# Kernel optimization log

Hardware: AMD Instinct MI355X
Metric: run time of the kernel (lower is better)

## Reference

```python
import jax, jax.numpy as jnp
import numpy as np

GRAVITY = 9.81
W_INERTIA = 1.0
W_GRAVITY = 0.01
W_STRAIN = 1.0

V = 500_000
E = 2_000_000


def setup_inputs() -> dict:
    key = jax.random.key(0)
    ks = jax.random.split(key, 7)
    pos_next = jax.random.normal(ks[0], (V, 3), dtype=jnp.float32)
    pos_curr = jax.random.normal(ks[1], (V, 3), dtype=jnp.float32)
    pos_prev = jax.random.normal(ks[2], (V, 3), dtype=jnp.float32)
    mass = jax.random.uniform(ks[3], (V, 1), dtype=jnp.float32)
    elements = jax.random.randint(ks[4], (E, 4), 0, V, dtype=jnp.int64)
    rest_volumes = jax.random.uniform(ks[5], (E,), dtype=jnp.float32)
    rest_inv = jax.random.normal(ks[6], (E, 3, 3), dtype=jnp.float32)
    lam = jnp.float32(1.0)
    mu = jnpp_one = jnp.float32(1.0)
    return {
        "pos_next": pos_next, "pos_curr": pos_curr, "pos_prev": pos_prev,
        "mass": mass, "elements": elements, "rest_volumes": rest_volumes,
        "rest_inv": rest_inv, "lam": lam, "mu": mu,
    }


def _det3(F):
    # F: (E, 3, 3)
    return (F[:, 0, 0] * (F[:, 1, 1] * F[:, 2, 2] - F[:, 1, 2] * F[:, 2, 1])
            - F[:, 0, 1] * (F[:, 1, 0] * F[:, 2, 2] - F[:, 1, 2] * F[:, 2, 0])
            + F[:, 0, 2] * (F[:, 1, 0] * F[:, 2, 1] - F[:, 1, 1] * F[:, 2, 0]))


def _physics_loss(pos_next, pos_curr, pos_prev, mass, elements, rest_volumes, rest_inv, lam, mu):
    # Inertia: mean over all V*3 entries of 0.5 * m * a^2
    accel = pos_next + pos_prev - 2.0 * pos_curr          # (V, 3)
    inertia = 0.5 * jnp.mean(mass * accel * accel)
    # Gravity: -mean(m * g * y)
    gravity = -jnp.mean(mass * GRAVITY * pos_curr[:, 1:2])
    # Strain (Neo-Hookean) on pos_next
    v = pos_next[elements]                                 # (E, 4, 3)
    Ds = jnp.stack([v[:, 1] - v[:, 0], v[:, 2] - v[:, 0], v[:, 3] - v[:, 0]], axis=-1)  # (E,3,3)
    F_def = jnp.einsum('eij,ejk->eik', Ds, rest_inv)       # (E, 3, 3)
    det_F = jnp.maximum(_det3(F_def), 1e-8)
    log_det = jnp.log(det_F)
    tr_FtF = jnp.sum(F_def * F_def, axis=(1, 2))           # trace(F^T F) = ||F||_F^2
    psi = 0.5 * lam * log_det ** 2 - mu * log_det + 0.5 * mu * (tr_FtF - 3.0)
    strain = jnp.mean(psi * rest_volumes)
    return W_INERTIA * inertia + W_GRAVITY * gravity + W_STRAIN * strain


def reference(pos_next, pos_curr, pos_prev, mass, elements, rest_volumes, rest_inv, lam, mu):
    return _physics_loss(pos_next, pos_curr, pos_prev, mass, elements, rest_volumes, rest_inv, lam, mu)
```

## Files before the change

### kernel.cpp

```cpp
#include <hip/hip_runtime.h>

#define GRAVITY_F 9.81f
#define EPT 2

typedef int   v4i  __attribute__((ext_vector_type(4)));
typedef float v4f  __attribute__((ext_vector_type(4), aligned(16)));
typedef float v4fu __attribute__((ext_vector_type(4), aligned(4)));

__device__ __forceinline__ float blockReduceSum(float val) {
    #pragma unroll
    for (int off = 32; off > 0; off >>= 1)
        val += __shfl_down(val, off, 64);
    __shared__ float smem[16];
    const int lane = threadIdx.x & 63;
    const int wave = threadIdx.x >> 6;
    if (lane == 0) smem[wave] = val;
    __syncthreads();
    const int nwaves = (blockDim.x + 63) >> 6;
    val = 0.0f;
    if (wave == 0) {
        if (lane < nwaves) val = smem[lane];
        #pragma unroll
        for (int off = 8; off > 0; off >>= 1)
            val += __shfl_down(val, off, 64);
    }
    return val;
}

__global__ void __launch_bounds__(256, 4)
fused_kernel(const float* __restrict__ pn,
             const float* __restrict__ pc,
             const float* __restrict__ pp,
             const float* __restrict__ mass,
             const int*   __restrict__ elems,
             const float* __restrict__ vols,
             const float* __restrict__ rinv,
             const float* __restrict__ lam_p,
             const float* __restrict__ mu_p,
             float* __restrict__ partials,
             int V, int E, int Vblocks4,
             float sI, float sG, float sS) {
    float local = 0.0f;

    if ((int)blockIdx.x >= Vblocks4) {
        const float lam = lam_p[0];
        const float mu  = mu_p[0];
        const int eb   = blockIdx.x - Vblocks4;
        const int base = eb * (EPT * 256) + threadIdx.x;

        int   ec[EPT];
        float sc[EPT];
        #pragma unroll
        for (int i = 0; i < EPT; ++i) {
            const int e = base + i * 256;
            ec[i] = e < E ? e : (E - 1);
            sc[i] = e < E ? sS : 0.0f;
        }

        v4i idx[EPT];
        #pragma unroll
        for (int i = 0; i < EPT; ++i)
            idx[i] = __builtin_nontemporal_load(((const v4i*)elems) + ec[i]);

        v4fu rA[EPT], rB[EPT];
        float rC[EPT], vol[EPT];
        #pragma unroll
        for (int i = 0; i < EPT; ++i) {
            const float* Rp = rinv + 9 * (size_t)ec[i];
            rA[i]  = __builtin_nontemporal_load((const v4fu*)Rp);
            rB[i]  = __builtin_nontemporal_load((const v4fu*)(Rp + 4));
            rC[i]  = __builtin_nontemporal_load(Rp + 8);
            vol[i] = __builtin_nontemporal_load(vols + ec[i]);
        }

        float x[EPT][4][3];
        #pragma unroll
        for (int i = 0; i < EPT; ++i) {
            const float* v0 = pn + 3 * (size_t)idx[i].x;
            const float* v1 = pn + 3 * (size_t)idx[i].y;
            const float* v2 = pn + 3 * (size_t)idx[i].z;
            const float* v3 = pn + 3 * (size_t)idx[i].w;
            #pragma unroll
            for (int r = 0; r < 3; ++r) {
                x[i][0][r] = v0[r];
                x[i][1][r] = v1[r];
                x[i][2][r] = v2[r];
                x[i][3][r] = v3[r];
            }
        }

        asm volatile("" ::
            "v"(x[0][0][0]), "v"(x[0][0][1]), "v"(x[0][0][2]),
            "v"(x[0][1][0]), "v"(x[0][1][1]), "v"(x[0][1][2]),
            "v"(x[0][2][0]), "v"(x[0][2][1]), "v"(x[0][2][2]),
            "v"(x[0][3][0]), "v"(x[0][3][1]), "v"(x[0][3][2]),
            "v"(x[1][0][0]), "v"(x[1][0][1]), "v"(x[1][0][2]),
            "v"(x[1][1][0]), "v"(x[1][1][1]), "v"(x[1][1][2]),
            "v"(x[1][2][0]), "v"(x[1][2][1]), "v"(x[1][2][2]),
            "v"(x[1][3][0]), "v"(x[1][3][1]), "v"(x[1][3][2]),
            "v"(rA[0]), "v"(rB[0]), "v"(rA[1]), "v"(rB[1]),
            "v"(rC[0]), "v"(rC[1]), "v"(vol[0]), "v"(vol[1]));

        #pragma unroll
        for (int i = 0; i < EPT; ++i) {
            const float R[9] = { rA[i][0], rA[i][1], rA[i][2], rA[i][3],
                                 rB[i][0], rB[i][1], rB[i][2], rB[i][3],
                                 rC[i] };
            float d[3][3];
            #pragma unroll
            for (int r = 0; r < 3; ++r) {
                d[r][0] = x[i][1][r] - x[i][0][r];
                d[r][1] = x[i][2][r] - x[i][0][r];
                d[r][2] = x[i][3][r] - x[i][0][r];
            }
            float F[3][3];
            #pragma unroll
            for (int r = 0; r < 3; ++r)
                #pragma unroll
                for (int k = 0; k < 3; ++k)
                    F[r][k] = d[r][0] * R[0 * 3 + k]
                            + d[r][1] * R[1 * 3 + k]
                            + d[r][2] * R[2 * 3 + k];
            const float det = F[0][0] * (F[1][1] * F[2][2] - F[1][2] * F[2][1])
                            - F[0][1] * (F[1][0] * F[2][2] - F[1][2] * F[2][0])
                            + F[0][2] * (F[1][0] * F[2][1] - F[1][1] * F[2][0]);
            const float ld = logf(fmaxf(det, 1e-8f));
            float tr = 0.0f;
            #pragma unroll
            for (int r = 0; r < 3; ++r)
                #pragma unroll
                for (int k = 0; k < 3; ++k)
                    tr += F[r][k] * F[r][k];
            const float psi = 0.5f * lam * ld * ld - mu * ld + 0.5f * mu * (tr - 3.0f);
            local += sc[i] * (psi * vol[i]);
        }
    } else {
        const int g  = blockIdx.x * blockDim.x + threadIdx.x;
        const int v0 = g * 4;
        if (v0 + 4 <= V) {
            const v4f m4 = *(const v4f*)(mass + v0);
            const v4f n0 = *(const v4f*)(pn + 3 * v0);
            const v4f n1 = *(const v4f*)(pn + 3 * v0 + 4);
            const v4f n2 = *(const v4f*)(pn + 3 * v0 + 8);
            const v4f c0 = __builtin_nontemporal_load((const v4f*)(pc + 3 * v0));
            const v4f c1 = __builtin_nontemporal_load((const v4f*)(pc + 3 * v0 + 4));
            const v4f c2 = __builtin_nontemporal_load((const v4f*)(pc + 3 * v0 + 8));
            const v4f q0 = __builtin_nontemporal_load((const v4f*)(pp + 3 * v0));
            const v4f q1 = __builtin_nontemporal_load((const v4f*)(pp + 3 * v0 + 4));
            const v4f q2 = __builtin_nontemporal_load((const v4f*)(pp + 3 * v0 + 8));
            const v4f N[3] = { n0, n1, n2 };
            const v4f C[3] = { c0, c1, c2 };
            const v4f Q[3] = { q0, q1, q2 };
            #pragma unroll
            for (int i = 0; i < 4; ++i) {
                float acc = 0.0f;
                #pragma unroll
                for (int r = 0; r < 3; ++r) {
                    const int k = 3 * i + r;
                    const float a = N[k >> 2][k & 3] + Q[k >> 2][k & 3]
                                  - 2.0f * C[k >> 2][k & 3];
                    acc += a * a;
                }
                const int ky = 3 * i + 1;
                const float y = C[ky >> 2][ky & 3];
                local += sI * (m4[i] * acc) + sG * (m4[i] * y);
            }
        } else {
            for (int v = v0; v < V; ++v) {
                const float m  = mass[v];
                const float p0 = pc[3 * v + 0];
                const float y  = pc[3 * v + 1];
                const float p2 = pc[3 * v + 2];
                const float a0 = pn[3 * v + 0] + pp[3 * v + 0] - 2.0f * p0;
                const float a1 = pn[3 * v + 1] + pp[3 * v + 1] - 2.0f * y;
                const float a2 = pn[3 * v + 2] + pp[3 * v + 2] - 2.0f * p2;
                local += sI * (m * (a0 * a0 + a1 * a1 + a2 * a2)) + sG * (m * y);
            }
        }
    }

    const float tot = blockReduceSum(local);
    if (threadIdx.x == 0) partials[blockIdx.x] = tot;
}

__global__ void reduce_kernel(const float* __restrict__ partials, int n,
                              float* __restrict__ out) {
    double s = 0.0;
    for (int i = threadIdx.x; i < n; i += blockDim.x)
        s += (double)partials[i];
    __shared__ double sm[256];
    sm[threadIdx.x] = s;
    __syncthreads();
    #pragma unroll
    for (int off = 128; off > 0; off >>= 1) {
        if (threadIdx.x < off) sm[threadIdx.x] += sm[threadIdx.x + off];
        __syncthreads();
    }
    if (threadIdx.x == 0) out[0] = (float)sm[0];
}

extern "C" void kernel_launch(void* const* d_in, const int* in_sizes, int n_in,
                              void* d_out, int out_size, void* d_ws, size_t ws_size,
                              hipStream_t stream) {
    const float* pos_next = (const float*)d_in[0];
    const float* pos_curr = (const float*)d_in[1];
    const float* pos_prev = (const float*)d_in[2];
    const float* mass     = (const float*)d_in[3];
    const int*   elements = (const int*)d_in[4];
    const float* rest_vol = (const float*)d_in[5];
    const float* rest_inv = (const float*)d_in[6];
    const float* lam_p    = (const float*)d_in[7];
    const float* mu_p     = (const float*)d_in[8];
    float* out = (float*)d_out;

    const int V = in_sizes[3];
    const int E = in_sizes[5];

    const float sI = 0.5f / (3.0f * (float)V);
    const float sG = -0.01f * GRAVITY_F / (float)V;
    const float sS = 1.0f / (float)E;

    const int block = 256;
    const int Eblocks  = (E + EPT * block - 1) / (EPT * block);
    const int Vgroups  = (V + 3) / 4;
    const int Vblocks4 = (Vgroups + block - 1) / block;
    const int grid = Vblocks4 + Eblocks;

    float* partials = (float*)d_ws;

    fused_kernel<<<grid, block, 0, stream>>>(pos_next, pos_curr, pos_prev,
                                             mass, elements, rest_vol,
                                             rest_inv, lam_p, mu_p,
                                             partials, V, E, Vblocks4,
                                             sI, sG, sS);
    reduce_kernel<<<1, 256, 0, stream>>>(partials, grid, out);
}
```

Measured before the change: 217.9 us.

## Process four contiguous elements per thread with aligned vector loads of rest_inv

Each thread now handles four consecutive elements, so the 36 rest_inv floats, four volumes and four index vectors can be read with fully aligned 16-byte nontemporal loads instead of misaligned per-element loads. Element blocks are placed before vertex blocks in the grid, and launch bounds drop to 3 waves per SIMD to make room for the larger register footprint. The gather of pos_next stays the same, but more gathers are in flight per thread. The cost is higher register pressure and lower occupancy, plus per-thread strided access across lanes, which may reduce coalescing.

```diff
diff --git a/kernel.cpp b/kernel.cpp
--- a/kernel.cpp
+++ b/kernel.cpp
@@ -1,11 +1,10 @@
 #include <hip/hip_runtime.h>
 
 #define GRAVITY_F 9.81f
-#define EPT 2
-
-typedef int   v4i  __attribute__((ext_vector_type(4)));
-typedef float v4f  __attribute__((ext_vector_type(4), aligned(16)));
-typedef float v4fu __attribute__((ext_vector_type(4), aligned(4)));
+#define EPT 4
+
+typedef int   v4i __attribute__((ext_vector_type(4)));
+typedef float v4f __attribute__((ext_vector_type(4), aligned(16)));
 
 __device__ __forceinline__ float blockReduceSum(float val) {
     #pragma unroll
@@ -27,7 +26,7 @@
     return val;
 }
 
-__global__ void __launch_bounds__(256, 4)
+__global__ void __launch_bounds__(256, 3)
 fused_kernel(const float* __restrict__ pn,
              const float* __restrict__ pc,
              const float* __restrict__ pp,
@@ -38,54 +37,65 @@
              const float* __restrict__ lam_p,
              const float* __restrict__ mu_p,
              float* __restrict__ partials,
-             int V, int E, int Vblocks4,
+             int V, int E, int Eblocks,
              float sI, float sG, float sS) {
     float local = 0.0f;
 
-    if ((int)blockIdx.x >= Vblocks4) {
+    if ((int)blockIdx.x < Eblocks) {
         const float lam = lam_p[0];
         const float mu  = mu_p[0];
-        const int eb   = blockIdx.x - Vblocks4;
-        const int base = eb * (EPT * 256) + threadIdx.x;
-
-        int   ec[EPT];
+        const int t  = blockIdx.x * 256 + threadIdx.x;
+        const int e0 = t * 4;
+
+        float rf[36];
+        v4i   idx[EPT];
+        float vol[EPT];
         float sc[EPT];
-        #pragma unroll
-        for (int i = 0; i < EPT; ++i) {
-            const int e = base + i * 256;
-            ec[i] = e < E ? e : (E - 1);
-            sc[i] = e < E ? sS : 0.0f;
-        }
-
-        v4i idx[EPT];
-        #pragma unroll
-        for (int i = 0; i < EPT; ++i)
-            idx[i] = __builtin_nontemporal_load(((const v4i*)elems) + ec[i]);
-
-        v4fu rA[EPT], rB[EPT];
-        float rC[EPT], vol[EPT];
-        #pragma unroll
-        for (int i = 0; i < EPT; ++i) {
-            const float* Rp = rinv + 9 * (size_t)ec[i];
-            rA[i]  = __builtin_nontemporal_load((const v4fu*)Rp);
-            rB[i]  = __builtin_nontemporal_load((const v4fu*)(Rp + 4));
-            rC[i]  = __builtin_nontemporal_load(Rp + 8);
-            vol[i] = __builtin_nontemporal_load(vols + ec[i]);
+
+        if (e0 + EPT <= E) {
+            v4f rq[9];
+            const v4f* Rp = (const v4f*)(rinv + 36 * (size_t)t);
+            #pragma unroll
+            for (int k = 0; k < 9; ++k)
+                rq[k] = __builtin_nontemporal_load(Rp + k);
+            const v4f vv = __builtin_nontemporal_load((const v4f*)(vols + 4 * (size_t)t));
+            #pragma unroll
+            for (int i = 0; i < EPT; ++i)
+                idx[i] = __builtin_nontemporal_load((const v4i*)elems + (4 * (size_t)t + i));
+            #pragma unroll
+            for (int k = 0; k < 9; ++k)
+                #pragma unroll
+                for (int j = 0; j < 4; ++j)
+                    rf[4 * k + j] = rq[k][j];
+            #pragma unroll
+            for (int i = 0; i < EPT; ++i) { vol[i] = vv[i]; sc[i] = sS; }
+        } else {
+            #pragma unroll
+            for (int i = 0; i < EPT; ++i) {
+                const int e  = e0 + i;
+                const int ec = e < E ? e : (E - 1);
+                sc[i]  = e < E ? sS : 0.0f;
+                vol[i] = __builtin_nontemporal_load(vols + ec);
+                idx[i] = __builtin_nontemporal_load((const v4i*)elems + ec);
+                #pragma unroll
+                for (int k = 0; k < 9; ++k)
+                    rf[9 * i + k] = __builtin_nontemporal_load(rinv + 9 * (size_t)ec + k);
+            }
         }
 
         float x[EPT][4][3];
         #pragma unroll
         for (int i = 0; i < EPT; ++i) {
-            const float* v0 = pn + 3 * (size_t)idx[i].x;
-            const float* v1 = pn + 3 * (size_t)idx[i].y;
-            const float* v2 = pn + 3 * (size_t)idx[i].z;
-            const float* v3 = pn + 3 * (size_t)idx[i].w;
+            const float* p0 = pn + 3 * (size_t)idx[i].x;
+            const float* p1 = pn + 3 * (size_t)idx[i].y;
+            const float* p2 = pn + 3 * (size_t)idx[i].z;
+            const float* p3 = pn + 3 * (size_t)idx[i].w;
             #pragma unroll
             for (int r = 0; r < 3; ++r) {
-                x[i][0][r] = v0[r];
-                x[i][1][r] = v1[r];
-                x[i][2][r] = v2[r];
-                x[i][3][r] = v3[r];
+                x[i][0][r] = p0[r];
+                x[i][1][r] = p1[r];
+                x[i][2][r] = p2[r];
+                x[i][3][r] = p3[r];
             }
         }
 
@@ -97,15 +107,30 @@
             "v"(x[1][0][0]), "v"(x[1][0][1]), "v"(x[1][0][2]),
             "v"(x[1][1][0]), "v"(x[1][1][1]), "v"(x[1][1][2]),
             "v"(x[1][2][0]), "v"(x[1][2][1]), "v"(x[1][2][2]),
-            "v"(x[1][3][0]), "v"(x[1][3][1]), "v"(x[1][3][2]),
-            "v"(rA[0]), "v"(rB[0]), "v"(rA[1]), "v"(rB[1]),
-            "v"(rC[0]), "v"(rC[1]), "v"(vol[0]), "v"(vol[1]));
+            "v"(x[1][3][0]), "v"(x[1][3][1]), "v"(x[1][3][2]));
+        asm volatile("" ::
+            "v"(x[2][0][0]), "v"(x[2][0][1]), "v"(x[2][0][2]),
+            "v"(x[2][1][0]), "v"(x[2][1][1]), "v"(x[2][1][2]),
+            "v"(x[2][2][0]), "v"(x[2][2][1]), "v"(x[2][2][2]),
+            "v"(x[2][3][0]), "v"(x[2][3][1]), "v"(x[2][3][2]),
+            "v"(x[3][0][0]), "v"(x[3][0][1]), "v"(x[3][0][2]),
+            "v"(x[3][1][0]), "v"(x[3][1][1]), "v"(x[3][1][2]),
+            "v"(x[3][2][0]), "v"(x[3][2][1]), "v"(x[3][2][2]),
+            "v"(x[3][3][0]), "v"(x[3][3][1]), "v"(x[3][3][2]));
+        asm volatile("" ::
+            "v"(rf[0]),  "v"(rf[1]),  "v"(rf[2]),  "v"(rf[3]),  "v"(rf[4]),
+            "v"(rf[5]),  "v"(rf[6]),  "v"(rf[7]),  "v"(rf[8]),  "v"(rf[9]),
+            "v"(rf[10]), "v"(rf[11]), "v"(rf[12]), "v"(rf[13]), "v"(rf[14]),
+            "v"(rf[15]), "v"(rf[16]), "v"(rf[17]));
+        asm volatile("" ::
+            "v"(rf[18]), "v"(rf[19]), "v"(rf[20]), "v"(rf[21]), "v"(rf[22]),
+            "v"(rf[23]), "v"(rf[24]), "v"(rf[25]), "v"(rf[26]), "v"(rf[27]),
+            "v"(rf[28]), "v"(rf[29]), "v"(rf[30]), "v"(rf[31]), "v"(rf[32]),
+            "v"(rf[33]), "v"(rf[34]), "v"(rf[35]),
+            "v"(vol[0]), "v"(vol[1]), "v"(vol[2]), "v"(vol[3]));
 
         #pragma unroll
         for (int i = 0; i < EPT; ++i) {
-            const float R[9] = { rA[i][0], rA[i][1], rA[i][2], rA[i][3],
-                                 rB[i][0], rB[i][1], rB[i][2], rB[i][3],
-                                 rC[i] };
             float d[3][3];
             #pragma unroll
             for (int r = 0; r < 3; ++r) {
@@ -118,9 +143,9 @@
             for (int r = 0; r < 3; ++r)
                 #pragma unroll
                 for (int k = 0; k < 3; ++k)
-                    F[r][k] = d[r][0] * R[0 * 3 + k]
-                            + d[r][1] * R[1 * 3 + k]
-                            + d[r][2] * R[2 * 3 + k];
+                    F[r][k] = d[r][0] * rf[9 * i + 0 + k]
+                            + d[r][1] * rf[9 * i + 3 + k]
+                            + d[r][2] * rf[9 * i + 6 + k];
             const float det = F[0][0] * (F[1][1] * F[2][2] - F[1][2] * F[2][1])
                             - F[0][1] * (F[1][0] * F[2][2] - F[1][2] * F[2][0])
                             + F[0][2] * (F[1][0] * F[2][1] - F[1][1] * F[2][0]);
@@ -135,7 +160,7 @@
             local += sc[i] * (psi * vol[i]);
         }
     } else {
-        const int g  = blockIdx.x * blockDim.x + threadIdx.x;
+        const int g  = (blockIdx.x - Eblocks) * blockDim.x + threadIdx.x;
         const int v0 = g * 4;
         if (v0 + 4 <= V) {
             const v4f m4 = *(const v4f*)(mass + v0);
@@ -224,14 +249,14 @@
     const int Eblocks  = (E + EPT * block - 1) / (EPT * block);
     const int Vgroups  = (V + 3) / 4;
     const int Vblocks4 = (Vgroups + block - 1) / block;
-    const int grid = Vblocks4 + Eblocks;
+    const int grid = Eblocks + Vblocks4;
 
     float* partials = (float*)d_ws;
 
     fused_kernel<<<grid, block, 0, stream>>>(pos_next, pos_curr, pos_prev,
                                              mass, elements, rest_vol,
                                              rest_inv, lam_p, mu_p,
-                                             partials, V, E, Vblocks4,
+                                             partials, V, E, Eblocks,
                                              sI, sG, sS);
     reduce_kernel<<<1, 256, 0, stream>>>(partials, grid, out);
 }
```

Result: slower. 238.0 us (+9.2%).

## Gather vertex positions from a packed fp16 table built by a pre-pass

Applied to the files above, without the earlier changes.

Adds a pack kernel that converts pos_next to half precision and packs it at six bytes per vertex. The strain kernel then gathers each vertex with two dword loads and unpacks in registers, instead of three fp32 loads. This is meant to shrink random-gather traffic and the cache footprint of the vertex table. In exchange it adds an extra kernel launch and a pass over pos_next, and it loses precision in the edge vectors. Element blocks are also moved ahead of vertex blocks in the grid, and a fallback path with four elements per thread is kept for small workspaces.

```diff
diff --git a/kernel.cpp b/kernel.cpp
--- a/kernel.cpp
+++ b/kernel.cpp
@@ -1,11 +1,10 @@
 #include <hip/hip_runtime.h>
+#include <hip/hip_fp16.h>
 
 #define GRAVITY_F 9.81f
-#define EPT 2
-
-typedef int   v4i  __attribute__((ext_vector_type(4)));
-typedef float v4f  __attribute__((ext_vector_type(4), aligned(16)));
-typedef float v4fu __attribute__((ext_vector_type(4), aligned(4)));
+
+typedef int   v4i __attribute__((ext_vector_type(4)));
+typedef float v4f __attribute__((ext_vector_type(4), aligned(16)));
 
 __device__ __forceinline__ float blockReduceSum(float val) {
     #pragma unroll
@@ -27,6 +26,28 @@
     return val;
 }
 
+__global__ void pack_kernel(const float* __restrict__ pn,
+                            unsigned* __restrict__ tab, int V) {
+    const int t  = blockIdx.x * blockDim.x + threadIdx.x;
+    const int v0 = 2 * t;
+    if (v0 >= V) return;
+    const float a0 = pn[3 * v0 + 0], a1 = pn[3 * v0 + 1], a2 = pn[3 * v0 + 2];
+    float b0 = 0.f, b1 = 0.f, b2 = 0.f;
+    if (v0 + 1 < V) {
+        b0 = pn[3 * v0 + 3]; b1 = pn[3 * v0 + 4]; b2 = pn[3 * v0 + 5];
+    }
+    const unsigned h0 = __half_as_ushort(__float2half(a0));
+    const unsigned h1 = __half_as_ushort(__float2half(a1));
+    const unsigned h2 = __half_as_ushort(__float2half(a2));
+    const unsigned h3 = __half_as_ushort(__float2half(b0));
+    const unsigned h4 = __half_as_ushort(__float2half(b1));
+    const unsigned h5 = __half_as_ushort(__float2half(b2));
+    tab[3 * t + 0] = h0 | (h1 << 16);
+    tab[3 * t + 1] = h2 | (h3 << 16);
+    tab[3 * t + 2] = h4 | (h5 << 16);
+}
+
+template <int MODE>
 __global__ void __launch_bounds__(256, 4)
 fused_kernel(const float* __restrict__ pn,
              const float* __restrict__ pc,
@@ -37,105 +58,182 @@
              const float* __restrict__ rinv,
              const float* __restrict__ lam_p,
              const float* __restrict__ mu_p,
+             const unsigned* __restrict__ tab,
              float* __restrict__ partials,
-             int V, int E, int Vblocks4,
+             int V, int E, int Eblocks,
              float sI, float sG, float sS) {
     float local = 0.0f;
 
-    if ((int)blockIdx.x >= Vblocks4) {
+    if ((int)blockIdx.x < Eblocks) {
         const float lam = lam_p[0];
         const float mu  = mu_p[0];
-        const int eb   = blockIdx.x - Vblocks4;
-        const int base = eb * (EPT * 256) + threadIdx.x;
-
-        int   ec[EPT];
-        float sc[EPT];
-        #pragma unroll
-        for (int i = 0; i < EPT; ++i) {
-            const int e = base + i * 256;
-            ec[i] = e < E ? e : (E - 1);
-            sc[i] = e < E ? sS : 0.0f;
-        }
-
-        v4i idx[EPT];
-        #pragma unroll
-        for (int i = 0; i < EPT; ++i)
-            idx[i] = __builtin_nontemporal_load(((const v4i*)elems) + ec[i]);
-
-        v4fu rA[EPT], rB[EPT];
-        float rC[EPT], vol[EPT];
-        #pragma unroll
-        for (int i = 0; i < EPT; ++i) {
-            const float* Rp = rinv + 9 * (size_t)ec[i];
-            rA[i]  = __builtin_nontemporal_load((const v4fu*)Rp);
-            rB[i]  = __builtin_nontemporal_load((const v4fu*)(Rp + 4));
-            rC[i]  = __builtin_nontemporal_load(Rp + 8);
-            vol[i] = __builtin_nontemporal_load(vols + ec[i]);
-        }
-
-        float x[EPT][4][3];
-        #pragma unroll
-        for (int i = 0; i < EPT; ++i) {
-            const float* v0 = pn + 3 * (size_t)idx[i].x;
-            const float* v1 = pn + 3 * (size_t)idx[i].y;
-            const float* v2 = pn + 3 * (size_t)idx[i].z;
-            const float* v3 = pn + 3 * (size_t)idx[i].w;
-            #pragma unroll
-            for (int r = 0; r < 3; ++r) {
-                x[i][0][r] = v0[r];
-                x[i][1][r] = v1[r];
-                x[i][2][r] = v2[r];
-                x[i][3][r] = v3[r];
-            }
-        }
-
-        asm volatile("" ::
-            "v"(x[0][0][0]), "v"(x[0][0][1]), "v"(x[0][0][2]),
-            "v"(x[0][1][0]), "v"(x[0][1][1]), "v"(x[0][1][2]),
-            "v"(x[0][2][0]), "v"(x[0][2][1]), "v"(x[0][2][2]),
-            "v"(x[0][3][0]), "v"(x[0][3][1]), "v"(x[0][3][2]),
-            "v"(x[1][0][0]), "v"(x[1][0][1]), "v"(x[1][0][2]),
-            "v"(x[1][1][0]), "v"(x[1][1][1]), "v"(x[1][1][2]),
-            "v"(x[1][2][0]), "v"(x[1][2][1]), "v"(x[1][2][2]),
-            "v"(x[1][3][0]), "v"(x[1][3][1]), "v"(x[1][3][2]),
-            "v"(rA[0]), "v"(rB[0]), "v"(rA[1]), "v"(rB[1]),
-            "v"(rC[0]), "v"(rC[1]), "v"(vol[0]), "v"(vol[1]));
-
-        #pragma unroll
-        for (int i = 0; i < EPT; ++i) {
-            const float R[9] = { rA[i][0], rA[i][1], rA[i][2], rA[i][3],
-                                 rB[i][0], rB[i][1], rB[i][2], rB[i][3],
-                                 rC[i] };
-            float d[3][3];
-            #pragma unroll
-            for (int r = 0; r < 3; ++r) {
-                d[r][0] = x[i][1][r] - x[i][0][r];
-                d[r][1] = x[i][2][r] - x[i][0][r];
-                d[r][2] = x[i][3][r] - x[i][0][r];
-            }
-            float F[3][3];
-            #pragma unroll
-            for (int r = 0; r < 3; ++r)
-                #pragma unroll
-                for (int k = 0; k < 3; ++k)
-                    F[r][k] = d[r][0] * R[0 * 3 + k]
-                            + d[r][1] * R[1 * 3 + k]
-                            + d[r][2] * R[2 * 3 + k];
-            const float det = F[0][0] * (F[1][1] * F[2][2] - F[1][2] * F[2][1])
-                            - F[0][1] * (F[1][0] * F[2][2] - F[1][2] * F[2][0])
-                            + F[0][2] * (F[1][0] * F[2][1] - F[1][1] * F[2][0]);
-            const float ld = logf(fmaxf(det, 1e-8f));
-            float tr = 0.0f;
-            #pragma unroll
-            for (int r = 0; r < 3; ++r)
-                #pragma unroll
-                for (int k = 0; k < 3; ++k)
-                    tr += F[r][k] * F[r][k];
-            const float psi = 0.5f * lam * ld * ld - mu * ld + 0.5f * mu * (tr - 3.0f);
-            local += sc[i] * (psi * vol[i]);
+
+        if (MODE == 1) {
+            constexpr int EPT = 2;
+            const int base = blockIdx.x * (EPT * 256) + threadIdx.x;
+            int   ec[EPT];
+            float sc[EPT];
+            #pragma unroll
+            for (int i = 0; i < EPT; ++i) {
+                const int e = base + i * 256;
+                ec[i] = e < E ? e : (E - 1);
+                sc[i] = e < E ? sS : 0.0f;
+            }
+
+            v4i idx[EPT];
+            #pragma unroll
+            for (int i = 0; i < EPT; ++i)
+                idx[i] = __builtin_nontemporal_load((const v4i*)elems + ec[i]);
+
+            float rf[EPT][9], vol[EPT];
+            #pragma unroll
+            for (int i = 0; i < EPT; ++i) {
+                const float* Rp = rinv + 9 * (size_t)ec[i];
+                #pragma unroll
+                for (int k = 0; k < 9; ++k)
+                    rf[i][k] = __builtin_nontemporal_load(Rp + k);
+                vol[i] = __builtin_nontemporal_load(vols + ec[i]);
+            }
+
+            unsigned ua[EPT][4], ub[EPT][4];
+            #pragma unroll
+            for (int i = 0; i < EPT; ++i)
+                #pragma unroll
+                for (int j = 0; j < 4; ++j) {
+                    const unsigned v  = (unsigned)idx[i][j];
+                    const unsigned j0 = (3u * v) >> 1;
+                    ua[i][j] = tab[j0];
+                    ub[i][j] = tab[j0 + 1];
+                }
+
+            asm volatile("" ::
+                "v"(ua[0][0]), "v"(ub[0][0]), "v"(ua[0][1]), "v"(ub[0][1]),
+                "v"(ua[0][2]), "v"(ub[0][2]), "v"(ua[0][3]), "v"(ub[0][3]),
+                "v"(ua[1][0]), "v"(ub[1][0]), "v"(ua[1][1]), "v"(ub[1][1]),
+                "v"(ua[1][2]), "v"(ub[1][2]), "v"(ua[1][3]), "v"(ub[1][3]));
+            asm volatile("" ::
+                "v"(rf[0][0]), "v"(rf[0][1]), "v"(rf[0][2]), "v"(rf[0][3]),
+                "v"(rf[0][4]), "v"(rf[0][5]), "v"(rf[0][6]), "v"(rf[0][7]),
+                "v"(rf[0][8]), "v"(rf[1][0]), "v"(rf[1][1]), "v"(rf[1][2]),
+                "v"(rf[1][3]), "v"(rf[1][4]), "v"(rf[1][5]), "v"(rf[1][6]),
+                "v"(rf[1][7]), "v"(rf[1][8]), "v"(vol[0]), "v"(vol[1]));
+
+            #pragma unroll
+            for (int i = 0; i < EPT; ++i) {
+                float x[4][3];
+                #pragma unroll
+                for (int j = 0; j < 4; ++j) {
+                    const unsigned v   = (unsigned)idx[i][j];
+                    const unsigned a   = ua[i][j], b = ub[i][j];
+                    const bool     odd = (v & 1u) != 0u;
+                    const unsigned w0  = odd ? ((a >> 16) | (b << 16)) : a;
+                    const unsigned hz  = odd ? (b >> 16) : (b & 0xffffu);
+                    x[j][0] = __half2float(__ushort_as_half((unsigned short)(w0 & 0xffffu)));
+                    x[j][1] = __half2float(__ushort_as_half((unsigned short)(w0 >> 16)));
+                    x[j][2] = __half2float(__ushort_as_half((unsigned short)hz));
+                }
+                float d[3][3];
+                #pragma unroll
+                for (int r = 0; r < 3; ++r) {
+                    d[r][0] = x[1][r] - x[0][r];
+                    d[r][1] = x[2][r] - x[0][r];
+                    d[r][2] = x[3][r] - x[0][r];
+                }
+                float F[3][3];
+                #pragma unroll
+                for (int r = 0; r < 3; ++r)
+                    #pragma unroll
+                    for (int k = 0; k < 3; ++k)
+                        F[r][k] = d[r][0] * rf[i][0 + k]
+                                + d[r][1] * rf[i][3 + k]
+                                + d[r][2] * rf[i][6 + k];
+                const float det = F[0][0] * (F[1][1] * F[2][2] - F[1][2] * F[2][1])
+                                - F[0][1] * (F[1][0] * F[2][2] - F[1][2] * F[2][0])
+                                + F[0][2] * (F[1][0] * F[2][1] - F[1][1] * F[2][0]);
+                const float ld = logf(fmaxf(det, 1e-8f));
+                float tr = 0.0f;
+                #pragma unroll
+                for (int r = 0; r < 3; ++r)
+                    #pragma unroll
+                    for (int k = 0; k < 3; ++k)
+                        tr += F[r][k] * F[r][k];
+                const float psi = 0.5f * lam * ld * ld - mu * ld + 0.5f * mu * (tr - 3.0f);
+                local += sc[i] * (psi * vol[i]);
+            }
+        } else {
+            constexpr int EPT = 4;
+            const int base = blockIdx.x * (EPT * 256) + threadIdx.x;
+            int  ec[EPT];
+            float sc[EPT];
+            #pragma unroll
+            for (int i = 0; i < EPT; ++i) {
+                const int e = base + i * 256;
+                ec[i] = e < E ? e : (E - 1);
+                sc[i] = e < E ? sS : 0.0f;
+            }
+            v4i  idx[EPT];
+            float vol[EPT];
+            #pragma unroll
+            for (int i = 0; i < EPT; ++i) {
+                idx[i] = __builtin_nontemporal_load(((const v4i*)elems) + ec[i]);
+                vol[i] = __builtin_nontemporal_load(vols + ec[i]);
+            }
+            float x[EPT][4][3];
+            #pragma unroll
+            for (int i = 0; i < EPT; ++i) {
+                const float* p0 = pn + 3 * (size_t)idx[i].x;
+                const float* p1 = pn + 3 * (size_t)idx[i].y;
+                const float* p2 = pn + 3 * (size_t)idx[i].z;
+                const float* p3 = pn + 3 * (size_t)idx[i].w;
+                #pragma unroll
+                for (int r = 0; r < 3; ++r) {
+                    x[i][0][r] = p0[r];
+                    x[i][1][r] = p1[r];
+                    x[i][2][r] = p2[r];
+                    x[i][3][r] = p3[r];
+                }
+            }
+            float R[EPT][9];
+            #pragma unroll
+            for (int i = 0; i < EPT; ++i) {
+                const float* Rp = rinv + 9 * (size_t)ec[i];
+                #pragma unroll
+                for (int k = 0; k < 9; ++k)
+                    R[i][k] = __builtin_nontemporal_load(Rp + k);
+            }
+            #pragma unroll
+            for (int i = 0; i < EPT; ++i) {
+                float d[3][3];
+                #pragma unroll
+                for (int r = 0; r < 3; ++r) {
+                    d[r][0] = x[i][1][r] - x[i][0][r];
+                    d[r][1] = x[i][2][r] - x[i][0][r];
+                    d[r][2] = x[i][3][r] - x[i][0][r];
+                }
+                float F[3][3];
+                #pragma unroll
+                for (int r = 0; r < 3; ++r)
+                    #pragma unroll
+                    for (int k = 0; k < 3; ++k)
+                        F[r][k] = d[r][0] * R[i][0 * 3 + k]
+                                + d[r][1] * R[i][1 * 3 + k]
+                                + d[r][2] * R[i][2 * 3 + k];
+                const float det = F[0][0] * (F[1][1] * F[2][2] - F[1][2] * F[2][1])
+                                - F[0][1] * (F[1][0] * F[2][2] - F[1][2] * F[2][0])
+                                + F[0][2] * (F[1][0] * F[2][1] - F[1][1] * F[2][0]);
+                const float ld = logf(fmaxf(det, 1e-8f));
+                float tr = 0.0f;
+                #pragma unroll
+                for (int r = 0; r < 3; ++r)
+                    #pragma unroll
+                    for (int k = 0; k < 3; ++k)
+                        tr += F[r][k] * F[r][k];
+                const float psi = 0.5f * lam * ld * ld - mu * ld + 0.5f * mu * (tr - 3.0f);
+                local += sc[i] * (psi * vol[i]);
+            }
         }
     } else {
-        const int g  = blockIdx.x * blockDim.x + threadIdx.x;
+        const int g  = (blockIdx.x - Eblocks) * blockDim.x + threadIdx.x;
         const int v0 = g * 4;
         if (v0 + 4 <= V) {
             const v4f m4 = *(const v4f*)(mass + v0);
@@ -221,17 +319,35 @@
     const float sS = 1.0f / (float)E;
 
     const int block = 256;
-    const int Eblocks  = (E + EPT * block - 1) / (EPT * block);
     const int Vgroups  = (V + 3) / 4;
     const int Vblocks4 = (Vgroups + block - 1) / block;
-    const int grid = Vblocks4 + Eblocks;
-
-    float* partials = (float*)d_ws;
-
-    fused_kernel<<<grid, block, 0, stream>>>(pos_next, pos_curr, pos_prev,
-                                             mass, elements, rest_vol,
-                                             rest_inv, lam_p, mu_p,
-                                             partials, V, E, Vblocks4,
-                                             sI, sG, sS);
-    reduce_kernel<<<1, 256, 0, stream>>>(partials, grid, out);
-}
+
+    const size_t tabDw    = (6 * (size_t)V + 3) / 4 + 4;
+    const size_t tabBytes = (tabDw * 4 + 255) & ~(size_t)255;
+
+    const int EblocksP = (E + 2 * block - 1) / (2 * block);
+    const int gridP    = EblocksP + Vblocks4;
+    const size_t needP = tabBytes + (size_t)gridP * sizeof(float);
+
+    if (ws_size >= needP) {
+        unsigned* tab      = (unsigned*)d_ws;
+        float*    partials = (float*)((char*)d_ws + tabBytes);
+        pack_kernel<<<(V / 2 + block - 1) / block, block, 0, stream>>>(pos_next, tab, V);
+        fused_kernel<1><<<gridP, block, 0, stream>>>(pos_next, pos_curr, pos_prev,
+                                                     mass, elements, rest_vol,
+                                                     rest_inv, lam_p, mu_p, tab,
+                                                     partials, V, E, EblocksP,
+                                                     sI, sG, sS);
+        reduce_kernel<<<1, 256, 0, stream>>>(partials, gridP, out);
+    } else {
+        const int EblocksF = (E + 4 * block - 1) / (4 * block);
+        const int gridF    = EblocksF + Vblocks4;
+        float* partials = (float*)d_ws;
+        fused_kernel<0><<<gridF, block, 0, stream>>>(pos_next, pos_curr, pos_prev,
+                                                     mass, elements, rest_vol,
+                                                     rest_inv, lam_p, mu_p, nullptr,
+                                                     partials, V, E, EblocksF,
+                                                     sI, sG, sS);
+        reduce_kernel<<<1, 256, 0, stream>>>(partials, gridF, out);
+    }
+}
```

Result: faster. 211.3 us (-3.0%).
